# Kernel optimization log

Hardware: AMD Instinct MI355X
Metric: run time of the kernel (lower is better)

Reference implementation:

```python
import jax, jax.numpy as jnp
import numpy as np

NUM_USERS = 100000
NUM_ITEMS = 100000
D = 128
L = 8
FV = 64
FH = 64
B = 8192
FC_IN = FV * D + FH * L  # 8704


def setup_inputs() -> dict:
    key = jax.random.key(0)
    ks = jax.random.split(key, 16)
    s = 0.05  # weight scale for sane magnitudes
    return {
        "user_id": jax.random.randint(ks[0], (B,), 0, NUM_USERS),
        "seq_L": jax.random.randint(ks[1], (B, L), 0, NUM_ITEMS),
        "item_id": jax.random.randint(ks[2], (B,), 0, NUM_ITEMS),
        "Q": jax.random.normal(ks[3], (NUM_ITEMS, D), jnp.float32) * s,
        "P": jax.random.normal(ks[4], (NUM_USERS, D), jnp.float32) * s,
        "Qp": jax.random.normal(ks[5], (NUM_ITEMS, 2 * D), jnp.float32) * s,
        "b_item": jax.random.normal(ks[6], (NUM_ITEMS,), jnp.float32) * s,
        "Wv": jax.random.normal(ks[7], (FV, L), jnp.float32) * s,
        "bv": jax.random.normal(ks[8], (FV,), jnp.float32) * s,
        "Wh": jax.random.normal(ks[9], (L, FH, L, D), jnp.float32) * s,
        "bh": jax.random.normal(ks[10], (L, FH), jnp.float32) * s,
        "Wfc": jax.random.normal(ks[11], (D, FC_IN), jnp.float32) * s,
        "bfc": jax.random.normal(ks[12], (D,), jnp.float32) * s,
    }


def reference(user_id, seq_L, item_id, Q, P, Qp, b_item, Wv, bv, Wh, bh, Wfc, bfc):
    # seq embeddings: [B, L, D]
    x = Q[seq_L]
    # vertical conv: kernel (L,1) -> out [B, Fv, D], then relu + flatten
    out_v = jax.nn.relu(jnp.einsum("bld,fl->bfd", x, Wv) + bv[None, :, None])
    out_v = out_v.reshape(out_v.shape[0], FV * D)  # [B, Fv*D]
    # horizontal conv blocks h = 1..L (static loop over kernel heights)
    h_feats = []
    for h in range(1, L + 1):
        w = Wh[h - 1, :, :h, :]  # [Fh, h, D]
        # sliding windows over sequence: [B, L-h+1, h, D]
        win = jnp.stack([x[:, j : j + h] for j in range(L - h + 1)], axis=1)
        o = jnp.einsum("bjhd,fhd->bjf", win, w) + bh[h - 1]  # [B, L-h+1, Fh]
        h_feats.append(jnp.max(jax.nn.relu(o), axis=1))  # [B, Fh]
    out_h = jnp.concatenate(h_feats, axis=1)  # [B, Fh*L]
    combined = jnp.concatenate([out_v, out_h], axis=1)  # [B, Fv*D + Fh*L]
    # (dropout p=0 / inference -> identity)
    z = jax.nn.relu(combined @ Wfc.T + bfc)  # [B, D]
    x2 = jnp.concatenate([z, P[user_id]], axis=1)  # [B, 2D]
    score = jnp.einsum("bd,bd->b", x2, Qp[item_id]) + b_item[item_id]
    return score
```

## Files before the change

kernel.cpp:

```cpp
#include <hip/hip_runtime.h>
#include <hip/hip_bf16.h>
#include <cstdint>
#include <cstddef>

typedef short bf16x8 __attribute__((ext_vector_type(8)));
typedef float f32x4  __attribute__((ext_vector_type(4)));

#define MFMA16(A, B, C) __builtin_amdgcn_mfma_f32_16x16x32_bf16(A, B, C, 0, 0, 0)

constexpr int XSTR = 1032;
constexpr int BSTR = 520;
constexpr size_t WS_FC   = (size_t)2176 * 1024;
constexpr size_t WS_BOTH = WS_FC + (size_t)576 * 1024;

__device__ __forceinline__ unsigned short f2bf(float x) {
    unsigned u = __float_as_uint(x);
    unsigned r = u + 0x7fffu + ((u >> 16) & 1u);
    return (unsigned short)(r >> 16);
}
__device__ __forceinline__ float bf2f(unsigned short h) {
    return __uint_as_float(((unsigned)h) << 16);
}
__device__ __forceinline__ unsigned pkbf(float a, float b) {
    __hip_bfloat162 h = __float22bfloat162_rn(make_float2(a, b));
    return *reinterpret_cast<unsigned*>(&h);
}
__device__ __forceinline__ bf16x8 load8_f32(const float* __restrict__ s) {
    float4 a = *(const float4*)s;
    float4 b = *(const float4*)(s + 4);
    bf16x8 r;
    r[0]=(short)f2bf(a.x); r[1]=(short)f2bf(a.y); r[2]=(short)f2bf(a.z); r[3]=(short)f2bf(a.w);
    r[4]=(short)f2bf(b.x); r[5]=(short)f2bf(b.y); r[6]=(short)f2bf(b.z); r[7]=(short)f2bf(b.w);
    return r;
}

template<int MODE>
__device__ __forceinline__ bf16x8 fc_bfrag(const unsigned short* __restrict__ wfcb,
                                           const float* __restrict__ Wfc,
                                           int kg, int ntile, int lane)
{
    if constexpr (MODE >= 1) {
        return *(const bf16x8*)(wfcb + (((size_t)(kg * 8 + ntile)) << 9) + lane * 8);
    } else {
        const float* s = Wfc + (size_t)(ntile * 16 + (lane & 15)) * 8704
                             + kg * 32 + (lane >> 4) * 8;
        return load8_f32(s);
    }
}
template<int MODE>
__device__ __forceinline__ bf16x8 wh_bfrag(const unsigned short* __restrict__ whb,
                                           const float* __restrict__ Wh,
                                           int H, int kstep, int ntile, int lane)
{
    if constexpr (MODE == 2) {
        return *(const bf16x8*)(whb +
            (((size_t)(8 * H * (H - 1) + kstep * 4 + ntile)) << 9) + lane * 8);
    } else {
        const int k = kstep * 32 + (lane >> 4) * 8;
        const float* s = Wh + ((((size_t)(H - 1) * 64 + ntile * 16 + (lane & 15)) * 8
                               + (k >> 7)) * 128 + (k & 127));
        return load8_f32(s);
    }
}

__global__ __launch_bounds__(256)
void caser_prep(const float* __restrict__ Wfc, const float* __restrict__ Wh,
                unsigned short* __restrict__ wfcb, unsigned short* __restrict__ whb,
                int nfrag)
{
    const int tid = blockIdx.x * 256 + threadIdx.x;
    const int lane = tid & 63, frag = tid >> 6;
    if (frag >= nfrag) return;
    if (frag < 2176) {
        const int kg = frag >> 3, nt = frag & 7;
        bf16x8 v = fc_bfrag<0>(nullptr, Wfc, kg, nt, lane);
        *(bf16x8*)(wfcb + ((size_t)frag << 9) + lane * 8) = v;
    } else {
        const int f2 = frag - 2176;
        int h = 1;
        while (f2 >= 8 * h * (h + 1)) ++h;
        const int fl = f2 - 8 * h * (h - 1);
        const int nt = fl & 3, kstep = fl >> 2;
        bf16x8 v = wh_bfrag<0>(nullptr, Wh, h, kstep, nt, lane);
        *(bf16x8*)(whb + ((size_t)f2 << 9) + lane * 8) = v;
    }
}

template<int H, int PP, int MODE>
__device__ __forceinline__ void hconv_compute(
    const unsigned short* __restrict__ xs,
    const unsigned short* __restrict__ whb, const float* __restrict__ Wh,
    const float* __restrict__ bh,
    int m, int n2, int lane, int laneA, float mx[2][4])
{
    constexpr int NJ = 9 - H;
    constexpr int NJS = (PP == 0) ? ((NJ + 1) / 2) : (NJ / 2);
    if constexpr (NJS > 0) {
        f32x4 C[NJS][2] = {};
        const unsigned short* xbase = xs + m * 16 * XSTR + laneA;
        #pragma unroll
        for (int kstep = 0; kstep < 4 * H; ++kstep) {
            const int hp = kstep >> 2, d0 = (kstep & 3) * 32;
            bf16x8 B0 = wh_bfrag<MODE>(whb, Wh, H, kstep, n2 * 2,     lane);
            bf16x8 B1 = wh_bfrag<MODE>(whb, Wh, H, kstep, n2 * 2 + 1, lane);
            #pragma unroll
            for (int idx = 0; idx < NJS; ++idx) {
                const int j = PP + 2 * idx;
                bf16x8 A = *(const bf16x8*)(xbase + (j + hp) * 128 + d0);
                C[idx][0] = MFMA16(A, B0, C[idx][0]);
                C[idx][1] = MFMA16(A, B1, C[idx][1]);
            }
        }
        #pragma unroll
        for (int nt = 0; nt < 2; ++nt) {
            const float bhv = bh[(H - 1) * 64 + n2 * 32 + nt * 16 + (lane & 15)];
            #pragma unroll
            for (int idx = 0; idx < NJS; ++idx)
                #pragma unroll
                for (int r = 0; r < 4; ++r)
                    mx[nt][r] = fmaxf(mx[nt][r], fmaxf(C[idx][nt][r] + bhv, 0.f));
        }
    }
}

template<int H, int MODE>
__device__ __forceinline__ void hstep(
    const unsigned short* __restrict__ xs, unsigned short* __restrict__ fb0,
    float* __restrict__ cand,
    const unsigned short* __restrict__ whb, const unsigned short* __restrict__ wfcb,
    const float* __restrict__ Wh, const float* __restrict__ Wfc,
    const float* __restrict__ bh,
    int t, int lane, int laneA, int laneB, int w, f32x4 (&FCC)[2][2])
{
    const int hm = w & 1, hn2 = (w >> 1) & 1, pj = w >> 2;
    const int kh = w & 1, ng = w >> 1;
    float mx[2][4] = {};
    if (pj == 0) hconv_compute<H, 0, MODE>(xs, whb, Wh, bh, hm, hn2, lane, laneA, mx);
    else         hconv_compute<H, 1, MODE>(xs, whb, Wh, bh, hm, hn2, lane, laneA, mx);
    #pragma unroll
    for (int nt = 0; nt < 2; ++nt)
        #pragma unroll
        for (int r = 0; r < 4; ++r)
            cand[pj * 2176 + (hm * 16 + (lane >> 4) * 4 + r) * 68 +
                 hn2 * 32 + nt * 16 + (lane & 15)] = mx[nt][r];
    __syncthreads();
    {
        const int s = t >> 4, f0 = (t & 15) * 4;
        float4 a = *(const float4*)&cand[s * 68 + f0];
        float4 b = *(const float4*)&cand[2176 + s * 68 + f0];
        uint2 pk;
        pk.x = pkbf(fmaxf(a.x, b.x), fmaxf(a.y, b.y));
        pk.y = pkbf(fmaxf(a.z, b.z), fmaxf(a.w, b.w));
        *(uint2*)(fb0 + s * BSTR + f0) = pk;
    }
    __syncthreads();
    {
        const int kg = 256 + (H - 1) * 2 + kh;
        bf16x8 B0 = fc_bfrag<MODE>(wfcb, Wfc, kg, ng * 2,     lane);
        bf16x8 B1 = fc_bfrag<MODE>(wfcb, Wfc, kg, ng * 2 + 1, lane);
        bf16x8 A0 = *(const bf16x8*)(fb0 + laneB + kh * 32);
        bf16x8 A1 = *(const bf16x8*)(fb0 + 16 * BSTR + laneB + kh * 32);
        FCC[0][0] = MFMA16(A0, B0, FCC[0][0]);
        FCC[0][1] = MFMA16(A0, B1, FCC[0][1]);
        FCC[1][0] = MFMA16(A1, B0, FCC[1][0]);
        FCC[1][1] = MFMA16(A1, B1, FCC[1][1]);
    }
    __syncthreads();
}

template<int MODE>
__global__ __launch_bounds__(512, 1)
void caser_main(const int* __restrict__ user_id,
                const int* __restrict__ seq,
                const int* __restrict__ item_id,
                const float* __restrict__ Q,
                const float* __restrict__ Pmat,
                const float* __restrict__ Qp,
                const float* __restrict__ b_item,
                const float* __restrict__ Wv,
                const float* __restrict__ bv,
                const float* __restrict__ Wh,
                const float* __restrict__ bh,
                const float* __restrict__ Wfc,
                const float* __restrict__ bfc,
                const unsigned short* __restrict__ wfcb,
                const unsigned short* __restrict__ whb,
                float* __restrict__ out)
{
    __shared__ unsigned short xs[32 * XSTR];
    __shared__ unsigned short fbuf[2 * 32 * BSTR];
    __shared__ float cand[2 * 32 * 68];
    __shared__ float wv_s[576];

    const int t = threadIdx.x;
    const int lane = t & 63;
    const int w = t >> 6;
    const int b0 = blockIdx.x * 32;
    const int laneA = (lane & 15) * XSTR + (lane >> 4) * 8;
    const int laneB = (lane & 15) * BSTR + (lane >> 4) * 8;

    for (int idx = t; idx < 576; idx += 512)
        wv_s[idx] = (idx < 512) ? Wv[idx] : bv[idx - 512];
    #pragma unroll 4
    for (int k = 0; k < 16; ++k) {
        const int idx = t + k * 512;
        const int i = idx & 31;
        const int l = (idx >> 5) & 7;
        const int s = idx >> 8;
        const int it = seq[(b0 + s) * 8 + l];
        float4 v = *(const float4*)(Q + (size_t)it * 128 + i * 4);
        uint2 pk;
        pk.x = pkbf(v.x, v.y);
        pk.y = pkbf(v.z, v.w);
        *(uint2*)(xs + s * XSTR + l * 128 + i * 4) = pk;
    }
    __syncthreads();

    const int sv = t & 31, dq = t >> 5;
    float xr[8][8];
    #pragma unroll
    for (int l = 0; l < 8; ++l) {
        bf16x8 v = *(const bf16x8*)(xs + sv * XSTR + l * 128 + dq * 8);
        #pragma unroll
        for (int i = 0; i < 8; ++i) xr[l][i] = bf2f((unsigned short)v[i]);
    }

    f32x4 FCC[2][2] = {};
    const int kh = w & 1, ng = w >> 1;

    uint4 vc[4];
    #define VCONV_HALF(hc_, dst_)                                              \
        {                                                                      \
            _Pragma("unroll")                                                  \
            for (int fl = 0; fl < 4; ++fl) {                                   \
                const int f = (hc_) * 4 + fl;                                  \
                const float bvv = wv_s[512 + f];                               \
                float acc[8];                                                  \
                _Pragma("unroll")                                              \
                for (int i = 0; i < 8; ++i) acc[i] = bvv;                      \
                _Pragma("unroll")                                              \
                for (int l = 0; l < 8; ++l) {                                  \
                    const float wl = wv_s[f * 8 + l];                          \
                    _Pragma("unroll")                                          \
                    for (int i = 0; i < 8; ++i)                                \
                        acc[i] = fmaf(xr[l][i], wl, acc[i]);                   \
                }                                                              \
                dst_[fl].x = pkbf(fmaxf(acc[0], 0.f), fmaxf(acc[1], 0.f));     \
                dst_[fl].y = pkbf(fmaxf(acc[2], 0.f), fmaxf(acc[3], 0.f));     \
                dst_[fl].z = pkbf(fmaxf(acc[4], 0.f), fmaxf(acc[5], 0.f));     \
                dst_[fl].w = pkbf(fmaxf(acc[6], 0.f), fmaxf(acc[7], 0.f));     \
            }                                                                  \
        }
    #define VSTORE(buf_, dst_)                                                 \
        {                                                                      \
            unsigned short* fb = fbuf + (buf_) * (32 * BSTR);                  \
            _Pragma("unroll")                                                  \
            for (int fl = 0; fl < 4; ++fl)                                     \
                *(uint4*)(fb + sv * BSTR + fl * 128 + dq * 8) = vc[fl];        \
        }

    VCONV_HALF(0, vc);
    VSTORE(0, vc);
    __syncthreads();

    #pragma unroll 2
    for (int hc = 0; hc < 16; ++hc) {
        uint4 nxt[4];
        if (hc < 15) VCONV_HALF(hc + 1, nxt);
        {
            const unsigned short* fb = fbuf + (hc & 1) * (32 * BSTR);
            #pragma unroll
            for (int ks = 0; ks < 8; ++ks) {
                const int kl = kh * 8 + ks;
                const int kg = hc * 16 + kl;
                bf16x8 B0 = fc_bfrag<MODE>(wfcb, Wfc, kg, ng * 2,     lane);
                bf16x8 B1 = fc_bfrag<MODE>(wfcb, Wfc, kg, ng * 2 + 1, lane);
                bf16x8 A0 = *(const bf16x8*)(fb + laneB + kl * 32);
                bf16x8 A1 = *(const bf16x8*)(fb + 16 * BSTR + laneB + kl * 32);
                FCC[0][0] = MFMA16(A0, B0, FCC[0][0]);
                FCC[0][1] = MFMA16(A0, B1, FCC[0][1]);
                FCC[1][0] = MFMA16(A1, B0, FCC[1][0]);
                FCC[1][1] = MFMA16(A1, B1, FCC[1][1]);
            }
        }
        if (hc < 15) {
            #pragma unroll
            for (int fl = 0; fl < 4; ++fl) vc[fl] = nxt[fl];
            VSTORE((hc + 1) & 1, vc);
        }
        __syncthreads();
    }
    #undef VCONV_HALF
    #undef VSTORE

    unsigned short* fb0 = fbuf;
    hstep<1, MODE>(xs, fb0, cand, whb, wfcb, Wh, Wfc, bh, t, lane, laneA, laneB, w, FCC);
    hstep<2, MODE>(xs, fb0, cand, whb, wfcb, Wh, Wfc, bh, t, lane, laneA, laneB, w, FCC);
    hstep<3, MODE>(xs, fb0, cand, whb, wfcb, Wh, Wfc, bh, t, lane, laneA, laneB, w, FCC);
    hstep<4, MODE>(xs, fb0, cand, whb, wfcb, Wh, Wfc, bh, t, lane, laneA, laneB, w, FCC);
    hstep<5, MODE>(xs, fb0, cand, whb, wfcb, Wh, Wfc, bh, t, lane, laneA, laneB, w, FCC);
    hstep<6, MODE>(xs, fb0, cand, whb, wfcb, Wh, Wfc, bh, t, lane, laneA, laneB, w, FCC);
    hstep<7, MODE>(xs, fb0, cand, whb, wfcb, Wh, Wfc, bh, t, lane, laneA, laneB, w, FCC);
    hstep<8, MODE>(xs, fb0, cand, whb, wfcb, Wh, Wfc, bh, t, lane, laneA, laneB, w, FCC);

    float* zbuf = cand;
    if (kh == 1) {
        #pragma unroll
        for (int m = 0; m < 2; ++m)
            #pragma unroll
            for (int nt = 0; nt < 2; ++nt)
                #pragma unroll
                for (int r = 0; r < 4; ++r)
                    zbuf[(m * 16 + (lane >> 4) * 4 + r) * 132 +
                         ng * 32 + nt * 16 + (lane & 15)] = FCC[m][nt][r];
    }
    __syncthreads();
    if (kh == 0) {
        #pragma unroll
        for (int m = 0; m < 2; ++m)
            #pragma unroll
            for (int nt = 0; nt < 2; ++nt) {
                const int o = ng * 32 + nt * 16 + (lane & 15);
                const float bfcv = bfc[o];
                #pragma unroll
                for (int r = 0; r < 4; ++r) {
                    const int idx = (m * 16 + (lane >> 4) * 4 + r) * 132 + o;
                    zbuf[idx] = fmaxf(zbuf[idx] + FCC[m][nt][r] + bfcv, 0.f);
                }
            }
    }
    __syncthreads();
    {
        const int s = t >> 4, l16 = t & 15, o0 = l16 * 8;
        const int b = b0 + s;
        const int item = item_id[b];
        const int user = user_id[b];
        const float* qp = Qp + (size_t)item * 256;
        const float* pu = Pmat + (size_t)user * 128;
        float acc2 = 0.f;
        #pragma unroll
        for (int i = 0; i < 8; ++i) acc2 = fmaf(zbuf[s * 132 + o0 + i], qp[o0 + i], acc2);
        #pragma unroll
        for (int i = 0; i < 8; ++i) acc2 = fmaf(pu[o0 + i], qp[128 + o0 + i], acc2);
        acc2 += __shfl_xor(acc2, 1, 16);
        acc2 += __shfl_xor(acc2, 2, 16);
        acc2 += __shfl_xor(acc2, 4, 16);
        acc2 += __shfl_xor(acc2, 8, 16);
        if (l16 == 0) out[b] = acc2 + b_item[item];
    }
}

extern "C" void kernel_launch(void* const* d_in, const int* in_sizes, int n_in,
                              void* d_out, int out_size, void* d_ws, size_t ws_size,
                              hipStream_t stream)
{
    const int*   user_id = (const int*)  d_in[0];
    const int*   seq     = (const int*)  d_in[1];
    const int*   item_id = (const int*)  d_in[2];
    const float* Q       = (const float*)d_in[3];
    const float* Pmat    = (const float*)d_in[4];
    const float* Qp      = (const float*)d_in[5];
    const float* b_item  = (const float*)d_in[6];
    const float* Wv      = (const float*)d_in[7];
    const float* bv      = (const float*)d_in[8];
    const float* Wh      = (const float*)d_in[9];
    const float* bh      = (const float*)d_in[10];
    const float* Wfc     = (const float*)d_in[11];
    const float* bfc     = (const float*)d_in[12];
    float* out = (float*)d_out;

    unsigned short* wfcb = (unsigned short*)d_ws;
    unsigned short* whb  = wfcb + WS_FC / 2;

    if (ws_size >= WS_BOTH) {
        hipLaunchKernelGGL(caser_prep, dim3(688), dim3(256), 0, stream,
                           Wfc, Wh, wfcb, whb, 2752);
        hipLaunchKernelGGL((caser_main<2>), dim3(256), dim3(512), 0, stream,
                           user_id, seq, item_id, Q, Pmat, Qp, b_item,
                           Wv, bv, Wh, bh, Wfc, bfc, wfcb, whb, out);
    } else if (ws_size >= WS_FC) {
        hipLaunchKernelGGL(caser_prep, dim3(544), dim3(256), 0, stream,
                           Wfc, Wh, wfcb, whb, 2176);
        hipLaunchKernelGGL((caser_main<1>), dim3(256), dim3(512), 0, stream,
                           user_id, seq, item_id, Q, Pmat, Qp, b_item,
                           Wv, bv, Wh, bh, Wfc, bfc, wfcb, whb, out);
    } else {
        hipLaunchKernelGGL((caser_main<0>), dim3(256), dim3(512), 0, stream,
                           user_id, seq, item_id, Q, Pmat, Qp, b_item,
                           Wv, bv, Wh, bh, Wfc, bfc,
                           (const unsigned short*)nullptr, (const unsigned short*)nullptr, out);
    }
}
```

Baseline: 92.85 us.

## Double block size to 1024 threads and defer horizontal-conv FC to one pass

Launches 1024-thread blocks (16 waves) instead of 512 and halves per-thread work in the vertical conv, the FC K-slices and the horizontal-conv N tiles. The horizontal-conv features are now collected for all eight heights into a feature buffer, and the FC contribution is done in one batch at the end instead of after each height, which removes one barrier per height. The four K-split FC partials are reduced through shared memory in the final scoring step, where bias and ReLU are also applied. The aim is more latency hiding and fewer syncs, at the cost of higher register pressure per block and extra shared-memory reduction traffic.

```diff
diff --git a/kernel.cpp b/kernel.cpp
--- a/kernel.cpp
+++ b/kernel.cpp
@@ -4,6 +4,7 @@
 #include <cstddef>
 
 typedef short bf16x8 __attribute__((ext_vector_type(8)));
+typedef short bf16x4 __attribute__((ext_vector_type(4)));
 typedef float f32x4  __attribute__((ext_vector_type(4)));
 
 #define MFMA16(A, B, C) __builtin_amdgcn_mfma_f32_16x16x32_bf16(A, B, C, 0, 0, 0)
@@ -91,85 +92,60 @@
     const unsigned short* __restrict__ xs,
     const unsigned short* __restrict__ whb, const float* __restrict__ Wh,
     const float* __restrict__ bh,
-    int m, int n2, int lane, int laneA, float mx[2][4])
+    int m, int nt4, int lane, int laneA, float mx[4])
 {
     constexpr int NJ = 9 - H;
     constexpr int NJS = (PP == 0) ? ((NJ + 1) / 2) : (NJ / 2);
     if constexpr (NJS > 0) {
-        f32x4 C[NJS][2] = {};
+        f32x4 C[NJS] = {};
         const unsigned short* xbase = xs + m * 16 * XSTR + laneA;
         #pragma unroll
         for (int kstep = 0; kstep < 4 * H; ++kstep) {
             const int hp = kstep >> 2, d0 = (kstep & 3) * 32;
-            bf16x8 B0 = wh_bfrag<MODE>(whb, Wh, H, kstep, n2 * 2,     lane);
-            bf16x8 B1 = wh_bfrag<MODE>(whb, Wh, H, kstep, n2 * 2 + 1, lane);
+            bf16x8 B = wh_bfrag<MODE>(whb, Wh, H, kstep, nt4, lane);
             #pragma unroll
             for (int idx = 0; idx < NJS; ++idx) {
                 const int j = PP + 2 * idx;
                 bf16x8 A = *(const bf16x8*)(xbase + (j + hp) * 128 + d0);
-                C[idx][0] = MFMA16(A, B0, C[idx][0]);
-                C[idx][1] = MFMA16(A, B1, C[idx][1]);
+                C[idx] = MFMA16(A, B, C[idx]);
             }
         }
-        #pragma unroll
-        for (int nt = 0; nt < 2; ++nt) {
-            const float bhv = bh[(H - 1) * 64 + n2 * 32 + nt * 16 + (lane & 15)];
-            #pragma unroll
-            for (int idx = 0; idx < NJS; ++idx)
-                #pragma unroll
-                for (int r = 0; r < 4; ++r)
-                    mx[nt][r] = fmaxf(mx[nt][r], fmaxf(C[idx][nt][r] + bhv, 0.f));
-        }
+        const float bhv = bh[(H - 1) * 64 + nt4 * 16 + (lane & 15)];
+        #pragma unroll
+        for (int idx = 0; idx < NJS; ++idx)
+            #pragma unroll
+            for (int r = 0; r < 4; ++r)
+                mx[r] = fmaxf(mx[r], fmaxf(C[idx][r] + bhv, 0.f));
     }
 }
 
 template<int H, int MODE>
 __device__ __forceinline__ void hstep(
-    const unsigned short* __restrict__ xs, unsigned short* __restrict__ fb0,
+    const unsigned short* __restrict__ xs, unsigned short* __restrict__ feat,
     float* __restrict__ cand,
-    const unsigned short* __restrict__ whb, const unsigned short* __restrict__ wfcb,
-    const float* __restrict__ Wh, const float* __restrict__ Wfc,
+    const unsigned short* __restrict__ whb, const float* __restrict__ Wh,
     const float* __restrict__ bh,
-    int t, int lane, int laneA, int laneB, int w, f32x4 (&FCC)[2][2])
-{
-    const int hm = w & 1, hn2 = (w >> 1) & 1, pj = w >> 2;
-    const int kh = w & 1, ng = w >> 1;
-    float mx[2][4] = {};
-    if (pj == 0) hconv_compute<H, 0, MODE>(xs, whb, Wh, bh, hm, hn2, lane, laneA, mx);
-    else         hconv_compute<H, 1, MODE>(xs, whb, Wh, bh, hm, hn2, lane, laneA, mx);
-    #pragma unroll
-    for (int nt = 0; nt < 2; ++nt)
-        #pragma unroll
-        for (int r = 0; r < 4; ++r)
-            cand[pj * 2176 + (hm * 16 + (lane >> 4) * 4 + r) * 68 +
-                 hn2 * 32 + nt * 16 + (lane & 15)] = mx[nt][r];
+    int t, int lane, int laneA, int hm, int hn4, int pj)
+{
+    float mx[4] = {};
+    if (pj == 0) hconv_compute<H, 0, MODE>(xs, whb, Wh, bh, hm, hn4, lane, laneA, mx);
+    else         hconv_compute<H, 1, MODE>(xs, whb, Wh, bh, hm, hn4, lane, laneA, mx);
+    #pragma unroll
+    for (int r = 0; r < 4; ++r)
+        cand[pj * 2176 + (hm * 16 + (lane >> 4) * 4 + r) * 68 +
+             hn4 * 16 + (lane & 15)] = mx[r];
     __syncthreads();
     {
-        const int s = t >> 4, f0 = (t & 15) * 4;
-        float4 a = *(const float4*)&cand[s * 68 + f0];
-        float4 b = *(const float4*)&cand[2176 + s * 68 + f0];
-        uint2 pk;
-        pk.x = pkbf(fmaxf(a.x, b.x), fmaxf(a.y, b.y));
-        pk.y = pkbf(fmaxf(a.z, b.z), fmaxf(a.w, b.w));
-        *(uint2*)(fb0 + s * BSTR + f0) = pk;
-    }
-    __syncthreads();
-    {
-        const int kg = 256 + (H - 1) * 2 + kh;
-        bf16x8 B0 = fc_bfrag<MODE>(wfcb, Wfc, kg, ng * 2,     lane);
-        bf16x8 B1 = fc_bfrag<MODE>(wfcb, Wfc, kg, ng * 2 + 1, lane);
-        bf16x8 A0 = *(const bf16x8*)(fb0 + laneB + kh * 32);
-        bf16x8 A1 = *(const bf16x8*)(fb0 + 16 * BSTR + laneB + kh * 32);
-        FCC[0][0] = MFMA16(A0, B0, FCC[0][0]);
-        FCC[0][1] = MFMA16(A0, B1, FCC[0][1]);
-        FCC[1][0] = MFMA16(A1, B0, FCC[1][0]);
-        FCC[1][1] = MFMA16(A1, B1, FCC[1][1]);
+        const int s = t >> 5, f0 = (t & 31) * 2;
+        float a0 = fmaxf(cand[s * 68 + f0],     cand[2176 + s * 68 + f0]);
+        float a1 = fmaxf(cand[s * 68 + f0 + 1], cand[2176 + s * 68 + f0 + 1]);
+        *(unsigned*)(feat + s * BSTR + (H - 1) * 64 + f0) = pkbf(a0, a1);
     }
     __syncthreads();
 }
 
 template<int MODE>
-__global__ __launch_bounds__(512, 1)
+__global__ __launch_bounds__(1024, 1)
 void caser_main(const int* __restrict__ user_id,
                 const int* __restrict__ seq,
                 const int* __restrict__ item_id,
@@ -198,12 +174,13 @@
     const int b0 = blockIdx.x * 32;
     const int laneA = (lane & 15) * XSTR + (lane >> 4) * 8;
     const int laneB = (lane & 15) * BSTR + (lane >> 4) * 8;
-
-    for (int idx = t; idx < 576; idx += 512)
-        wv_s[idx] = (idx < 512) ? Wv[idx] : bv[idx - 512];
-    #pragma unroll 4
-    for (int k = 0; k < 16; ++k) {
-        const int idx = t + k * 512;
+    const int kh = w & 3, ng = w >> 2;
+    const int hm = w & 1, hn4 = (w >> 1) & 3, pj = (w >> 3) & 1;
+
+    if (t < 576) wv_s[t] = (t < 512) ? Wv[t] : bv[t - 512];
+    #pragma unroll
+    for (int k = 0; k < 8; ++k) {
+        const int idx = t + k * 1024;
         const int i = idx & 31;
         const int l = (idx >> 5) & 7;
         const int s = idx >> 8;
@@ -217,61 +194,58 @@
     __syncthreads();
 
     const int sv = t & 31, dq = t >> 5;
-    float xr[8][8];
+    float xr[8][4];
     #pragma unroll
     for (int l = 0; l < 8; ++l) {
-        bf16x8 v = *(const bf16x8*)(xs + sv * XSTR + l * 128 + dq * 8);
-        #pragma unroll
-        for (int i = 0; i < 8; ++i) xr[l][i] = bf2f((unsigned short)v[i]);
+        bf16x4 v = *(const bf16x4*)(xs + sv * XSTR + l * 128 + dq * 4);
+        #pragma unroll
+        for (int i = 0; i < 4; ++i) xr[l][i] = bf2f((unsigned short)v[i]);
     }
 
     f32x4 FCC[2][2] = {};
-    const int kh = w & 1, ng = w >> 1;
-
-    uint4 vc[4];
+
+    uint2 vc[4];
     #define VCONV_HALF(hc_, dst_)                                              \
         {                                                                      \
             _Pragma("unroll")                                                  \
             for (int fl = 0; fl < 4; ++fl) {                                   \
                 const int f = (hc_) * 4 + fl;                                  \
                 const float bvv = wv_s[512 + f];                               \
-                float acc[8];                                                  \
+                float acc[4];                                                  \
                 _Pragma("unroll")                                              \
-                for (int i = 0; i < 8; ++i) acc[i] = bvv;                      \
+                for (int i = 0; i < 4; ++i) acc[i] = bvv;                      \
                 _Pragma("unroll")                                              \
                 for (int l = 0; l < 8; ++l) {                                  \
                     const float wl = wv_s[f * 8 + l];                          \
                     _Pragma("unroll")                                          \
-                    for (int i = 0; i < 8; ++i)                                \
+                    for (int i = 0; i < 4; ++i)                                \
                         acc[i] = fmaf(xr[l][i], wl, acc[i]);                   \
                 }                                                              \
                 dst_[fl].x = pkbf(fmaxf(acc[0], 0.f), fmaxf(acc[1], 0.f));     \
                 dst_[fl].y = pkbf(fmaxf(acc[2], 0.f), fmaxf(acc[3], 0.f));     \
-                dst_[fl].z = pkbf(fmaxf(acc[4], 0.f), fmaxf(acc[5], 0.f));     \
-                dst_[fl].w = pkbf(fmaxf(acc[6], 0.f), fmaxf(acc[7], 0.f));     \
             }                                                                  \
         }
-    #define VSTORE(buf_, dst_)                                                 \
+    #define VSTORE(buf_)                                                       \
         {                                                                      \
             unsigned short* fb = fbuf + (buf_) * (32 * BSTR);                  \
             _Pragma("unroll")                                                  \
             for (int fl = 0; fl < 4; ++fl)                                     \
-                *(uint4*)(fb + sv * BSTR + fl * 128 + dq * 8) = vc[fl];        \
+                *(uint2*)(fb + sv * BSTR + fl * 128 + dq * 4) = vc[fl];        \
         }
 
     VCONV_HALF(0, vc);
-    VSTORE(0, vc);
+    VSTORE(0);
     __syncthreads();
 
     #pragma unroll 2
     for (int hc = 0; hc < 16; ++hc) {
-        uint4 nxt[4];
+        uint2 nxt[4];
         if (hc < 15) VCONV_HALF(hc + 1, nxt);
         {
             const unsigned short* fb = fbuf + (hc & 1) * (32 * BSTR);
             #pragma unroll
-            for (int ks = 0; ks < 8; ++ks) {
-                const int kl = kh * 8 + ks;
+            for (int ks = 0; ks < 4; ++ks) {
+                const int kl = kh * 4 + ks;
                 const int kg = hc * 16 + kl;
                 bf16x8 B0 = fc_bfrag<MODE>(wfcb, Wfc, kg, ng * 2,     lane);
                 bf16x8 B1 = fc_bfrag<MODE>(wfcb, Wfc, kg, ng * 2 + 1, lane);
@@ -286,52 +260,49 @@
         if (hc < 15) {
             #pragma unroll
             for (int fl = 0; fl < 4; ++fl) vc[fl] = nxt[fl];
-            VSTORE((hc + 1) & 1, vc);
+            VSTORE((hc + 1) & 1);
         }
         __syncthreads();
     }
     #undef VCONV_HALF
     #undef VSTORE
 
-    unsigned short* fb0 = fbuf;
-    hstep<1, MODE>(xs, fb0, cand, whb, wfcb, Wh, Wfc, bh, t, lane, laneA, laneB, w, FCC);
-    hstep<2, MODE>(xs, fb0, cand, whb, wfcb, Wh, Wfc, bh, t, lane, laneA, laneB, w, FCC);
-    hstep<3, MODE>(xs, fb0, cand, whb, wfcb, Wh, Wfc, bh, t, lane, laneA, laneB, w, FCC);
-    hstep<4, MODE>(xs, fb0, cand, whb, wfcb, Wh, Wfc, bh, t, lane, laneA, laneB, w, FCC);
-    hstep<5, MODE>(xs, fb0, cand, whb, wfcb, Wh, Wfc, bh, t, lane, laneA, laneB, w, FCC);
-    hstep<6, MODE>(xs, fb0, cand, whb, wfcb, Wh, Wfc, bh, t, lane, laneA, laneB, w, FCC);
-    hstep<7, MODE>(xs, fb0, cand, whb, wfcb, Wh, Wfc, bh, t, lane, laneA, laneB, w, FCC);
-    hstep<8, MODE>(xs, fb0, cand, whb, wfcb, Wh, Wfc, bh, t, lane, laneA, laneB, w, FCC);
-
-    float* zbuf = cand;
-    if (kh == 1) {
-        #pragma unroll
-        for (int m = 0; m < 2; ++m)
-            #pragma unroll
-            for (int nt = 0; nt < 2; ++nt)
-                #pragma unroll
-                for (int r = 0; r < 4; ++r)
-                    zbuf[(m * 16 + (lane >> 4) * 4 + r) * 132 +
-                         ng * 32 + nt * 16 + (lane & 15)] = FCC[m][nt][r];
-    }
-    __syncthreads();
-    if (kh == 0) {
-        #pragma unroll
-        for (int m = 0; m < 2; ++m)
-            #pragma unroll
-            for (int nt = 0; nt < 2; ++nt) {
-                const int o = ng * 32 + nt * 16 + (lane & 15);
-                const float bfcv = bfc[o];
-                #pragma unroll
-                for (int r = 0; r < 4; ++r) {
-                    const int idx = (m * 16 + (lane >> 4) * 4 + r) * 132 + o;
-                    zbuf[idx] = fmaxf(zbuf[idx] + FCC[m][nt][r] + bfcv, 0.f);
-                }
-            }
-    }
+    unsigned short* feat = fbuf;
+    hstep<1, MODE>(xs, feat, cand, whb, Wh, bh, t, lane, laneA, hm, hn4, pj);
+    hstep<2, MODE>(xs, feat, cand, whb, Wh, bh, t, lane, laneA, hm, hn4, pj);
+    hstep<3, MODE>(xs, feat, cand, whb, Wh, bh, t, lane, laneA, hm, hn4, pj);
+    hstep<4, MODE>(xs, feat, cand, whb, Wh, bh, t, lane, laneA, hm, hn4, pj);
+    hstep<5, MODE>(xs, feat, cand, whb, Wh, bh, t, lane, laneA, hm, hn4, pj);
+    hstep<6, MODE>(xs, feat, cand, whb, Wh, bh, t, lane, laneA, hm, hn4, pj);
+    hstep<7, MODE>(xs, feat, cand, whb, Wh, bh, t, lane, laneA, hm, hn4, pj);
+    hstep<8, MODE>(xs, feat, cand, whb, Wh, bh, t, lane, laneA, hm, hn4, pj);
+
+    #pragma unroll
+    for (int kgi = 0; kgi < 4; ++kgi) {
+        const int kloc = kh * 4 + kgi;
+        const int kg = 256 + kloc;
+        bf16x8 B0 = fc_bfrag<MODE>(wfcb, Wfc, kg, ng * 2,     lane);
+        bf16x8 B1 = fc_bfrag<MODE>(wfcb, Wfc, kg, ng * 2 + 1, lane);
+        bf16x8 A0 = *(const bf16x8*)(feat + laneB + kloc * 32);
+        bf16x8 A1 = *(const bf16x8*)(feat + 16 * BSTR + laneB + kloc * 32);
+        FCC[0][0] = MFMA16(A0, B0, FCC[0][0]);
+        FCC[0][1] = MFMA16(A0, B1, FCC[0][1]);
+        FCC[1][0] = MFMA16(A1, B0, FCC[1][0]);
+        FCC[1][1] = MFMA16(A1, B1, FCC[1][1]);
+    }
+
+    float* zbuf4 = (float*)xs;
+    #pragma unroll
+    for (int m = 0; m < 2; ++m)
+        #pragma unroll
+        for (int nt = 0; nt < 2; ++nt)
+            #pragma unroll
+            for (int r = 0; r < 4; ++r)
+                zbuf4[kh * (32 * 132) + (m * 16 + (lane >> 4) * 4 + r) * 132 +
+                      ng * 32 + nt * 16 + (lane & 15)] = FCC[m][nt][r];
     __syncthreads();
     {
-        const int s = t >> 4, l16 = t & 15, o0 = l16 * 8;
+        const int s = t >> 5, l32 = t & 31, o0 = l32 * 4;
         const int b = b0 + s;
         const int item = item_id[b];
         const int user = user_id[b];
@@ -339,14 +310,24 @@
         const float* pu = Pmat + (size_t)user * 128;
         float acc2 = 0.f;
         #pragma unroll
-        for (int i = 0; i < 8; ++i) acc2 = fmaf(zbuf[s * 132 + o0 + i], qp[o0 + i], acc2);
-        #pragma unroll
-        for (int i = 0; i < 8; ++i) acc2 = fmaf(pu[o0 + i], qp[128 + o0 + i], acc2);
-        acc2 += __shfl_xor(acc2, 1, 16);
-        acc2 += __shfl_xor(acc2, 2, 16);
-        acc2 += __shfl_xor(acc2, 4, 16);
-        acc2 += __shfl_xor(acc2, 8, 16);
-        if (l16 == 0) out[b] = acc2 + b_item[item];
+        for (int i = 0; i < 4; ++i) {
+            float z = zbuf4[s * 132 + o0 + i]
+                    + zbuf4[1 * (32 * 132) + s * 132 + o0 + i]
+                    + zbuf4[2 * (32 * 132) + s * 132 + o0 + i]
+                    + zbuf4[3 * (32 * 132) + s * 132 + o0 + i]
+                    + bfc[o0 + i];
+            z = fmaxf(z, 0.f);
+            acc2 = fmaf(z, qp[o0 + i], acc2);
+        }
+        #pragma unroll
+        for (int i = 0; i < 4; ++i)
+            acc2 = fmaf(pu[o0 + i], qp[128 + o0 + i], acc2);
+        acc2 += __shfl_xor(acc2, 1, 32);
+        acc2 += __shfl_xor(acc2, 2, 32);
+        acc2 += __shfl_xor(acc2, 4, 32);
+        acc2 += __shfl_xor(acc2, 8, 32);
+        acc2 += __shfl_xor(acc2, 16, 32);
+        if (l32 == 0) out[b] = acc2 + b_item[item];
     }
 }
 
@@ -375,17 +356,17 @@
     if (ws_size >= WS_BOTH) {
         hipLaunchKernelGGL(caser_prep, dim3(688), dim3(256), 0, stream,
                            Wfc, Wh, wfcb, whb, 2752);
-        hipLaunchKernelGGL((caser_main<2>), dim3(256), dim3(512), 0, stream,
+        hipLaunchKernelGGL((caser_main<2>), dim3(256), dim3(1024), 0, stream,
                            user_id, seq, item_id, Q, Pmat, Qp, b_item,
                            Wv, bv, Wh, bh, Wfc, bfc, wfcb, whb, out);
     } else if (ws_size >= WS_FC) {
         hipLaunchKernelGGL(caser_prep, dim3(544), dim3(256), 0, stream,
                            Wfc, Wh, wfcb, whb, 2176);
-        hipLaunchKernelGGL((caser_main<1>), dim3(256), dim3(512), 0, stream,
+        hipLaunchKernelGGL((caser_main<1>), dim3(256), dim3(1024), 0, stream,
                            user_id, seq, item_id, Q, Pmat, Qp, b_item,
                            Wv, bv, Wh, bh, Wfc, bfc, wfcb, whb, out);
     } else {
-        hipLaunchKernelGGL((caser_main<0>), dim3(256), dim3(512), 0, stream,
+        hipLaunchKernelGGL((caser_main<0>), dim3(256), dim3(1024), 0, stream,
                            user_id, seq, item_id, Q, Pmat, Qp, b_item,
                            Wv, bv, Wh, bh, Wfc, bfc,
                            (const unsigned short*)nullptr, (const unsigned short*)nullptr, out);
```

Result: faster. 85.87 us (-7.5%).
